# Performance work log

Measured on AMD Instinct MI355X. Metric: run time of the kernel, lower is better.

## Reference

```python
import jax, jax.numpy as jnp
import numpy as np
import math

B, N, DIM, H, D = 2, 2048, 1024, 16, 64
EXPECTED_K = 1.0
LAYERSCALE_INIT = 0.001
EPS = 1e-6  # flax LayerNorm default


def layer_norm(x, scale, bias):
    mu = jnp.mean(x, axis=-1, keepdims=True)
    var = jnp.mean((x - mu) ** 2, axis=-1, keepdims=True)
    return (x - mu) * jax.lax.rsqrt(var + EPS) * scale + bias


def setup_inputs() -> dict:
    key = jax.random.key(0)
    ks = jax.random.split(key, 8)
    s = DIM ** -0.5
    x = jax.random.normal(ks[0], (B, N, DIM), jnp.float32)
    Wq = jax.random.normal(ks[1], (DIM, H * D), jnp.float32) * s
    Wk = jax.random.normal(ks[2], (DIM, H * D), jnp.float32) * s
    Wv = jax.random.normal(ks[3], (DIM, H * D), jnp.float32) * s
    Wo = jax.random.normal(ks[4], (H * D, DIM), jnp.float32) * ((H * D) ** -0.5)
    e = EXPECTED_K / N
    init_bias = jnp.full((1, 1, 1, 1), math.log(e / (1.0 - e)), jnp.float32)
    return {
        'x': x,
        'Wq': Wq, 'bq': jnp.zeros((H * D,), jnp.float32),
        'Wk': Wk, 'bk': jnp.zeros((H * D,), jnp.float32),
        'Wv': Wv, 'bv': jnp.zeros((H * D,), jnp.float32),
        'qn_scale': jnp.ones((D,), jnp.float32), 'qn_bias': jnp.zeros((D,), jnp.float32),
        'kn_scale': jnp.ones((D,), jnp.float32), 'kn_bias': jnp.zeros((D,), jnp.float32),
        'init_bias': init_bias,
        'Wo': Wo, 'bo': jnp.zeros((DIM,), jnp.float32),
        'gamma': jnp.full((DIM,), LAYERSCALE_INIT, jnp.float32),
    }


def reference(x, Wq, bq, Wk, bk, Wv, bv, qn_scale, qn_bias, kn_scale, kn_bias,
              init_bias, Wo, bo, gamma):
    Bv, Nv, _ = x.shape
    q = (x @ Wq + bq).reshape(Bv, Nv, H, D)
    k = (x @ Wk + bk).reshape(Bv, Nv, H, D)
    v = (x @ Wv + bv).reshape(Bv, Nv, H, D)
    q = layer_norm(q, qn_scale, qn_bias)
    k = layer_norm(k, kn_scale, kn_bias)
    q = jnp.swapaxes(q, 1, 2)  # [B,H,N,D]
    k = jnp.swapaxes(k, 1, 2)
    v = jnp.swapaxes(v, 1, 2)
    # NOTE: original code computes scale = head_dim**-0.5 but never applies it.
    attn_logits = jnp.einsum('bhid,bhjd->bhij', q, k)
    attn_weights = jax.nn.sigmoid(attn_logits + init_bias)
    out = jnp.einsum('bhij,bhjd->bhid', attn_weights, v)
    out = jnp.swapaxes(out, 1, 2).reshape(Bv, Nv, H * D)
    out = out @ Wo + bo
    return out * gamma
```

## Files before the change

kernel.cpp:

```cpp
#include <hip/hip_runtime.h>

#define DEV static __device__ __forceinline__

typedef __bf16 bf16x8 __attribute__((ext_vector_type(8)));
typedef __bf16 bf16x4 __attribute__((ext_vector_type(4)));
typedef float f32x4 __attribute__((ext_vector_type(4)));
typedef float f32x16 __attribute__((ext_vector_type(16)));
typedef unsigned int uint4v __attribute__((ext_vector_type(4)));
typedef unsigned short ushort4v __attribute__((ext_vector_type(4)));
using u16 = unsigned short;

#define NN 2048
#define DIMD 1024

DEV u16 f2bf(float f) {
    __bf16 b = (__bf16)f;
    return __builtin_bit_cast(u16, b);
}
DEV float bf2f(u16 s) {
    unsigned u = ((unsigned)s) << 16;
    return __builtin_bit_cast(float, u);
}
DEV bf16x8 load16(const u16* p) { return __builtin_bit_cast(bf16x8, *(const uint4v*)p); }
DEV f32x4 mfma16(bf16x8 a, bf16x8 b, f32x4 c) {
    return __builtin_amdgcn_mfma_f32_16x16x32_bf16(a, b, c, 0, 0, 0);
}
DEV f32x16 mfma32(bf16x8 a, bf16x8 b, f32x16 c) {
    return __builtin_amdgcn_mfma_f32_32x32x16_bf16(a, b, c, 0, 0, 0);
}
DEV void gl_lds16(const u16* g, u16* l) {
    __builtin_amdgcn_global_load_lds((const __attribute__((address_space(1))) void*)g,
                                     (__attribute__((address_space(3))) void*)l, 16, 0, 0);
}


__global__ __launch_bounds__(256) void k_prep(const float* __restrict__ x,
                                              const float* __restrict__ s0,
                                              const float* __restrict__ s1,
                                              const float* __restrict__ s2,
                                              const float* __restrict__ s3,
                                              u16* __restrict__ xb,
                                              u16* __restrict__ wqkv_t,
                                              u16* __restrict__ wo_t) {
    __shared__ float tile[32][33];
    const int z = blockIdx.z;
    if (z < 4) {
        const float* src = (z == 0) ? s0 : (z == 1) ? s1 : (z == 2) ? s2 : s3;
        u16* dst = (z < 3) ? (wqkv_t + (size_t)z * 1024 * 1024) : wo_t;
        int tx = threadIdx.x & 31, ty = threadIdx.x >> 5;
        int kb = blockIdx.y * 32, nb = blockIdx.x * 32;
#pragma unroll
        for (int j = 0; j < 4; ++j)
            tile[ty + 8 * j][tx] = src[(size_t)(kb + ty + 8 * j) * 1024 + nb + tx];
        __syncthreads();
#pragma unroll
        for (int j = 0; j < 4; ++j)
            dst[(size_t)(nb + ty + 8 * j) * 1024 + kb + tx] = f2bf(tile[tx][ty + 8 * j]);
    } else {
        const int bidx = blockIdx.y * 32 + blockIdx.x;
#pragma unroll
        for (int q = 0; q < 4; ++q) {
            int i = bidx * 1024 + q * 256 + threadIdx.x;
            float4 v = ((const float4*)x)[i];
            ushort4v o;
            o[0] = f2bf(v.x); o[1] = f2bf(v.y); o[2] = f2bf(v.z); o[3] = f2bf(v.w);
            *(ushort4v*)(xb + (size_t)i * 4) = o;
        }
    }
}

__global__ __launch_bounds__(256) void k_gemm_qkv(const u16* __restrict__ A,
                                                  const u16* __restrict__ Bt,
                                                  const float* __restrict__ bq,
                                                  const float* __restrict__ bk,
                                                  const float* __restrict__ bv,
                                                  const float* __restrict__ qs,
                                                  const float* __restrict__ qb,
                                                  const float* __restrict__ ks,
                                                  const float* __restrict__ kb_,
                                                  u16* __restrict__ Qf,
                                                  u16* __restrict__ Kf,
                                                  u16* __restrict__ Vf) {
    __shared__ u16 As[128 * 64];
    __shared__ u16 Bs[128 * 64];
    const int K = 1024;
    const int m0 = blockIdx.x * 128, n0 = blockIdx.y * 128;
    const int tid = threadIdx.x;
    const int lane = tid & 63, w = tid >> 6;
    const int wr = w >> 1, wc = w & 1;
    const int li = lane & 15, g = lane >> 4;
    const int l7 = li & 7;

    f32x4 acc[4][4] = {};

    const int lr = lane >> 3;
    const int lc = (lane & 7) ^ lr;
    const u16* gA = A + (size_t)(m0 + w * 8 + lr) * K + lc * 8;
    const u16* gB = Bt + (size_t)(n0 + w * 8 + lr) * K + lc * 8;
    u16* lA = &As[w * 512];
    u16* lB = &Bs[w * 512];

    for (int k0 = 0; k0 < K; k0 += 64) {
        __syncthreads();
#pragma unroll
        for (int i = 0; i < 4; ++i) {
            gl_lds16(gA + (size_t)(i * 32) * K + k0, lA + i * 2048);
            gl_lds16(gB + (size_t)(i * 32) * K + k0, lB + i * 2048);
        }
        asm volatile("s_waitcnt vmcnt(0)" ::: "memory");
        __syncthreads();
        bf16x8 af[4][2], bfv[4][2];
#pragma unroll
        for (int mi = 0; mi < 4; ++mi) {
            const int row = wr * 64 + mi * 16 + li;
#pragma unroll
            for (int s = 0; s < 2; ++s)
                af[mi][s] = load16(&As[row * 64 + (((s * 4 + g) ^ l7) * 8)]);
        }
#pragma unroll
        for (int ni = 0; ni < 4; ++ni) {
            const int row = wc * 64 + ni * 16 + li;
#pragma unroll
            for (int s = 0; s < 2; ++s)
                bfv[ni][s] = load16(&Bs[row * 64 + (((s * 4 + g) ^ l7) * 8)]);
        }
#pragma unroll
        for (int mi = 0; mi < 4; ++mi)
#pragma unroll
            for (int ni = 0; ni < 4; ++ni) {
                acc[mi][ni] = mfma16(af[mi][0], bfv[ni][0], acc[mi][ni]);
                acc[mi][ni] = mfma16(af[mi][1], bfv[ni][1], acc[mi][ni]);
            }
    }

    const int col0 = n0 + wc * 64;
    const int seg = col0 >> 10;
    const int hcol = col0 & 1023;
    const int h = hcol >> 6;

    if (seg < 2) {
        const float* S = (seg == 0) ? qs : ks;
        const float* Bb = (seg == 0) ? qb : kb_;
        const float* bias = (seg == 0) ? bq : bk;
        u16* dst = (seg == 0) ? Qf : Kf;
        const float sc = (seg == 0) ? -1.44269504f : 1.0f;
        float lnS[4], lnB[4], bv4[4];
#pragma unroll
        for (int ni = 0; ni < 4; ++ni) {
            int d = ni * 16 + li;
            lnS[ni] = S[d] * sc; lnB[ni] = Bb[d] * sc; bv4[ni] = bias[hcol + d];
        }
#pragma unroll
        for (int mi = 0; mi < 4; ++mi) {
#pragma unroll
            for (int r = 0; r < 4; ++r) {
                float v0 = acc[mi][0][r] + bv4[0];
                float v1 = acc[mi][1][r] + bv4[1];
                float v2 = acc[mi][2][r] + bv4[2];
                float v3 = acc[mi][3][r] + bv4[3];
                float s1 = v0 + v1 + v2 + v3;
                float s2 = v0 * v0 + v1 * v1 + v2 * v2 + v3 * v3;
#pragma unroll
                for (int o = 1; o < 16; o <<= 1) {
                    s1 += __shfl_xor(s1, o);
                    s2 += __shfl_xor(s2, o);
                }
                float mu = s1 * (1.0f / 64.0f);
                float var = s2 * (1.0f / 64.0f) - mu * mu;
                float rsv = rsqrtf(var + 1e-6f);
                int row = m0 + wr * 64 + mi * 16 + 4 * g + r;
                int bseq = row >> 11, n = row & 2047;
                size_t base = ((size_t)(bseq * 16 + h)) * 131072 +
                              ((size_t)(n >> 5) * 4) * 512 + (size_t)(n & 31) * 8 +
                              (li >> 3) * 256 + (li & 7);
                dst[base + 0 * 512] = f2bf((v0 - mu) * rsv * lnS[0] + lnB[0]);
                dst[base + 1 * 512] = f2bf((v1 - mu) * rsv * lnS[1] + lnB[1]);
                dst[base + 2 * 512] = f2bf((v2 - mu) * rsv * lnS[2] + lnB[2]);
                dst[base + 3 * 512] = f2bf((v3 - mu) * rsv * lnS[3] + lnB[3]);
            }
        }
    } else {
        float bv4[4];
#pragma unroll
        for (int ni = 0; ni < 4; ++ni) bv4[ni] = bv[hcol + ni * 16 + li];
#pragma unroll
        for (int mi = 0; mi < 4; ++mi) {
#pragma unroll
            for (int r = 0; r < 4; ++r) {
                int row = m0 + wr * 64 + mi * 16 + 4 * g + r;
                int bseq = row >> 11, j = row & 2047;
                size_t vb_ = ((size_t)(bseq * 16 + h)) * 131072 +
                             ((size_t)((j >> 5) * 4 + ((j >> 4) & 1))) * 512 +
                             (size_t)(((j >> 3) & 1) * 32) * 8 + (j & 7);
#pragma unroll
                for (int ni = 0; ni < 4; ++ni)
                    Vf[vb_ + (ni >> 1) * 1024 + ((ni & 1) * 16 + li) * 8] =
                        f2bf(acc[mi][ni][r] + bv4[ni]);
            }
        }
    }
}

__global__ __launch_bounds__(256) void k_gemm_out(const u16* __restrict__ A,
                                                  const u16* __restrict__ Bt,
                                                  const float* __restrict__ bias,
                                                  const float* __restrict__ gamma,
                                                  float* __restrict__ out) {
    __shared__ u16 As[128 * 64];
    __shared__ u16 Bs[64 * 64];
    const int K = 1024, ldc = 1024;
    const int m0 = blockIdx.x * 128, n0 = blockIdx.y * 64;
    const int tid = threadIdx.x;
    const int lane = tid & 63, w = tid >> 6;
    const int wr = w >> 1, wc = w & 1;
    const int li = lane & 15, g = lane >> 4;
    const int l7 = li & 7;

    f32x4 acc[4][2] = {};

    const int lr = lane >> 3;
    const int lc = (lane & 7) ^ lr;
    const u16* gA = A + (size_t)(m0 + w * 8 + lr) * K + lc * 8;
    const u16* gB = Bt + (size_t)(n0 + w * 8 + lr) * K + lc * 8;
    u16* lA = &As[w * 512];
    u16* lB = &Bs[w * 512];

    for (int k0 = 0; k0 < K; k0 += 64) {
        __syncthreads();
#pragma unroll
        for (int i = 0; i < 4; ++i)
            gl_lds16(gA + (size_t)(i * 32) * K + k0, lA + i * 2048);
#pragma unroll
        for (int i = 0; i < 2; ++i)
            gl_lds16(gB + (size_t)(i * 32) * K + k0, lB + i * 2048);
        asm volatile("s_waitcnt vmcnt(0)" ::: "memory");
        __syncthreads();
        bf16x8 af[4][2], bfv[2][2];
#pragma unroll
        for (int mi = 0; mi < 4; ++mi) {
            const int row = wr * 64 + mi * 16 + li;
#pragma unroll
            for (int s = 0; s < 2; ++s)
                af[mi][s] = load16(&As[row * 64 + (((s * 4 + g) ^ l7) * 8)]);
        }
#pragma unroll
        for (int ni = 0; ni < 2; ++ni) {
            const int row = wc * 32 + ni * 16 + li;
#pragma unroll
            for (int s = 0; s < 2; ++s)
                bfv[ni][s] = load16(&Bs[row * 64 + (((s * 4 + g) ^ l7) * 8)]);
        }
#pragma unroll
        for (int mi = 0; mi < 4; ++mi)
#pragma unroll
            for (int ni = 0; ni < 2; ++ni) {
                acc[mi][ni] = mfma16(af[mi][0], bfv[ni][0], acc[mi][ni]);
                acc[mi][ni] = mfma16(af[mi][1], bfv[ni][1], acc[mi][ni]);
            }
    }

#pragma unroll
    for (int mi = 0; mi < 4; ++mi) {
        int row = m0 + wr * 64 + mi * 16 + 4 * g;
#pragma unroll
        for (int ni = 0; ni < 2; ++ni) {
            int col = n0 + wc * 32 + ni * 16 + li;
            float bv_ = bias[col], gv = gamma[col];
            f32x4 v = acc[mi][ni];
#pragma unroll
            for (int r = 0; r < 4; ++r)
                out[(size_t)(row + r) * ldc + col] = (v[r] + bv_) * gv;
        }
    }
}

__global__ __launch_bounds__(256, 2) void k_attn(const u16* __restrict__ Qf,
                                                 const u16* __restrict__ Kf,
                                                 const u16* __restrict__ Vf,
                                                 const float* __restrict__ ib,
                                                 u16* __restrict__ attn_out) {
    __shared__ float red[2][64][65];
    const int bid = blockIdx.x;
    const int xcd = bid & 7, idx = bid >> 3;
    const int bh = xcd * 4 + (idx >> 5);
    const int iblk = idx & 31;
    const int b = bh >> 4, h = bh & 15;
    const int tid = threadIdx.x;
    const int jq = tid >> 6, lane = tid & 63;
    const int l32 = lane & 31, hi = lane >> 5;
    const float c0 = -ib[0] * 1.44269504f;
    const u16* Qb = Qf + (size_t)bh * 131072;
    const u16* Kb = Kf + (size_t)bh * 131072;
    const u16* Vb = Vf + (size_t)bh * 131072;
    const int it0 = iblk * 2;

    bf16x8 qf[2][4];
#pragma unroll
    for (int t = 0; t < 2; ++t)
#pragma unroll
        for (int s = 0; s < 4; ++s)
            qf[t][s] = load16(Qb + ((size_t)((it0 + t) * 4 + s)) * 512 + lane * 8);

    f32x16 accO[2][2] = {};
    const u16* kb0 = Kb + (size_t)(jq * 16) * 2048;
    const u16* vb0 = Vb + (size_t)(jq * 16) * 2048;

    f32x16 cinit;
#pragma unroll
    for (int r = 0; r < 16; ++r) cinit[r] = c0;

    bf16x8 kf[2][4], vf[2][2][2];
#pragma unroll
    for (int s = 0; s < 4; ++s) kf[0][s] = load16(kb0 + s * 512 + lane * 8);
#pragma unroll
    for (int s = 0; s < 4; ++s) kf[1][s] = load16(kb0 + 2048 + s * 512 + lane * 8);
#pragma unroll
    for (int db = 0; db < 2; ++db)
#pragma unroll
        for (int js = 0; js < 2; ++js)
            vf[0][db][js] = load16(vb0 + (db * 2 + js) * 512 + lane * 8);
    f32x16 sa0 = cinit, sa1;
#pragma unroll
    for (int s = 0; s < 4; ++s) sa0 = mfma32(kf[0][s], qf[0][s], sa0);

#pragma unroll 2
    for (int jt = 0; jt < 16; ++jt) {
        const int cur = jt & 1, nxt = cur ^ 1;
        if (jt < 15) {
            const u16* vbn = vb0 + (size_t)(jt + 1) * 2048;
#pragma unroll
            for (int db = 0; db < 2; ++db)
#pragma unroll
                for (int js = 0; js < 2; ++js)
                    vf[nxt][db][js] = load16(vbn + (db * 2 + js) * 512 + lane * 8);
        }
        __builtin_amdgcn_s_setprio(1);
        sa1 = cinit;
#pragma unroll
        for (int s = 0; s < 4; ++s) sa1 = mfma32(kf[cur][s], qf[1][s], sa1);
        __builtin_amdgcn_s_setprio(0);
        if (jt < 14) {
            const u16* kbn = kb0 + (size_t)(jt + 2) * 2048;
#pragma unroll
            for (int s = 0; s < 4; ++s) kf[cur][s] = load16(kbn + s * 512 + lane * 8);
        }
        bf16x8 p00, p01;
        {
            float p[16];
#pragma unroll
            for (int r = 0; r < 16; ++r) {
                float e = __builtin_amdgcn_exp2f(sa0[r]);
                p[r] = __builtin_amdgcn_rcpf(1.0f + e);
            }
            unsigned wd[8];
#pragma unroll
            for (int u2 = 0; u2 < 8; ++u2) {
                unsigned r_;
                asm("v_cvt_pk_bf16_f32 %0, %1, %2"
                    : "=v"(r_) : "v"(p[2 * u2]), "v"(p[2 * u2 + 1]));
                wd[u2] = r_;
            }
            asm("v_permlane32_swap_b32 %0, %1" : "+v"(wd[0]), "+v"(wd[2]));
            asm("v_permlane32_swap_b32 %0, %1" : "+v"(wd[1]), "+v"(wd[3]));
            asm("v_permlane32_swap_b32 %0, %1" : "+v"(wd[4]), "+v"(wd[6]));
            asm("v_permlane32_swap_b32 %0, %1" : "+v"(wd[5]), "+v"(wd[7]));
            uint4v u0 = {wd[0], wd[1], wd[2], wd[3]};
            uint4v u1 = {wd[4], wd[5], wd[6], wd[7]};
            p00 = __builtin_bit_cast(bf16x8, u0);
            p01 = __builtin_bit_cast(bf16x8, u1);
        }
        __builtin_amdgcn_s_setprio(1);
        accO[0][0] = mfma32(vf[cur][0][0], p00, accO[0][0]);
        accO[0][0] = mfma32(vf[cur][0][1], p01, accO[0][0]);
        accO[0][1] = mfma32(vf[cur][1][0], p00, accO[0][1]);
        accO[0][1] = mfma32(vf[cur][1][1], p01, accO[0][1]);
        if (jt < 15) {
            sa0 = cinit;
#pragma unroll
            for (int s = 0; s < 4; ++s) sa0 = mfma32(kf[nxt][s], qf[0][s], sa0);
        }
        __builtin_amdgcn_s_setprio(0);
        bf16x8 p10, p11;
        {
            float p[16];
#pragma unroll
            for (int r = 0; r < 16; ++r) {
                float e = __builtin_amdgcn_exp2f(sa1[r]);
                p[r] = __builtin_amdgcn_rcpf(1.0f + e);
            }
            unsigned wd[8];
#pragma unroll
            for (int u2 = 0; u2 < 8; ++u2) {
                unsigned r_;
                asm("v_cvt_pk_bf16_f32 %0, %1, %2"
                    : "=v"(r_) : "v"(p[2 * u2]), "v"(p[2 * u2 + 1]));
                wd[u2] = r_;
            }
            asm("v_permlane32_swap_b32 %0, %1" : "+v"(wd[0]), "+v"(wd[2]));
            asm("v_permlane32_swap_b32 %0, %1" : "+v"(wd[1]), "+v"(wd[3]));
            asm("v_permlane32_swap_b32 %0, %1" : "+v"(wd[4]), "+v"(wd[6]));
            asm("v_permlane32_swap_b32 %0, %1" : "+v"(wd[5]), "+v"(wd[7]));
            uint4v u0 = {wd[0], wd[1], wd[2], wd[3]};
            uint4v u1 = {wd[4], wd[5], wd[6], wd[7]};
            p10 = __builtin_bit_cast(bf16x8, u0);
            p11 = __builtin_bit_cast(bf16x8, u1);
        }
        __builtin_amdgcn_s_setprio(1);
        accO[1][0] = mfma32(vf[cur][0][0], p10, accO[1][0]);
        accO[1][0] = mfma32(vf[cur][0][1], p11, accO[1][0]);
        accO[1][1] = mfma32(vf[cur][1][0], p10, accO[1][1]);
        accO[1][1] = mfma32(vf[cur][1][1], p11, accO[1][1]);
        __builtin_amdgcn_s_setprio(0);
    }

    if (jq & 1) {
#pragma unroll
        for (int t = 0; t < 2; ++t)
#pragma unroll
            for (int db = 0; db < 2; ++db)
#pragma unroll
                for (int r = 0; r < 16; ++r)
                    red[jq >> 1][t * 32 + l32][db * 32 + (r & 3) + 8 * (r >> 2) + 4 * hi] =
                        accO[t][db][r];
    }
    __syncthreads();
    if (!(jq & 1)) {
#pragma unroll
        for (int t = 0; t < 2; ++t)
#pragma unroll
            for (int db = 0; db < 2; ++db)
#pragma unroll
                for (int r = 0; r < 16; ++r)
                    accO[t][db][r] +=
                        red[jq >> 1][t * 32 + l32][db * 32 + (r & 3) + 8 * (r >> 2) + 4 * hi];
    }
    __syncthreads();
    if (jq == 2) {
#pragma unroll
        for (int t = 0; t < 2; ++t)
#pragma unroll
            for (int db = 0; db < 2; ++db)
#pragma unroll
                for (int r = 0; r < 16; ++r)
                    red[0][t * 32 + l32][db * 32 + (r & 3) + 8 * (r >> 2) + 4 * hi] =
                        accO[t][db][r];
    }
    __syncthreads();
    if (jq == 0) {
#pragma unroll
        for (int t = 0; t < 2; ++t)
#pragma unroll
            for (int db = 0; db < 2; ++db)
#pragma unroll
                for (int r = 0; r < 16; ++r)
                    accO[t][db][r] +=
                        red[0][t * 32 + l32][db * 32 + (r & 3) + 8 * (r >> 2) + 4 * hi];
#pragma unroll
        for (int t = 0; t < 2; ++t) {
            const int i = it0 * 32 + t * 32 + l32;
#pragma unroll
            for (int db = 0; db < 2; ++db)
#pragma unroll
                for (int q = 0; q < 4; ++q) {
                    int d = db * 32 + 8 * q + 4 * hi;
                    bf16x4 o4;
#pragma unroll
                    for (int r = 0; r < 4; ++r) o4[r] = (__bf16)accO[t][db][4 * q + r];
                    *(bf16x4*)&attn_out[(size_t)(b * NN + i) * 1024 + h * 64 + d] = o4;
                }
        }
    }
}


extern "C" void kernel_launch(void* const* d_in, const int* in_sizes, int n_in,
                              void* d_out, int out_size, void* d_ws, size_t ws_size,
                              hipStream_t stream) {
    (void)in_sizes; (void)n_in; (void)out_size; (void)ws_size;
    const float* x     = (const float*)d_in[0];
    const float* Wq    = (const float*)d_in[1];
    const float* bq    = (const float*)d_in[2];
    const float* Wk    = (const float*)d_in[3];
    const float* bk    = (const float*)d_in[4];
    const float* Wv    = (const float*)d_in[5];
    const float* bv    = (const float*)d_in[6];
    const float* qn_s  = (const float*)d_in[7];
    const float* qn_b  = (const float*)d_in[8];
    const float* kn_s  = (const float*)d_in[9];
    const float* kn_b  = (const float*)d_in[10];
    const float* ib    = (const float*)d_in[11];
    const float* Wo    = (const float*)d_in[12];
    const float* bo    = (const float*)d_in[13];
    const float* gamma = (const float*)d_in[14];
    float* out = (float*)d_out;

    char* ws = (char*)d_ws;
    size_t off = 0;
    auto alloc = [&](size_t bytes) -> void* {
        void* p = ws + off;
        off += (bytes + 255) & ~(size_t)255;
        return p;
    };
    u16* xb       = (u16*)alloc((size_t)4096 * 1024 * 2);
    u16* wqkv_t   = (u16*)alloc((size_t)3072 * 1024 * 2);
    u16* wo_t     = (u16*)alloc((size_t)1024 * 1024 * 2);
    u16* Qf       = (u16*)alloc((size_t)32 * 131072 * 2);
    u16* Kf       = (u16*)alloc((size_t)32 * 131072 * 2);
    u16* Vf       = (u16*)alloc((size_t)32 * 131072 * 2);
    u16* attn_out = (u16*)alloc((size_t)4096 * 1024 * 2);

    k_prep<<<dim3(32, 32, 5), 256, 0, stream>>>(x, Wq, Wk, Wv, Wo, xb, wqkv_t, wo_t);
    k_gemm_qkv<<<dim3(32, 24), 256, 0, stream>>>(xb, wqkv_t, bq, bk, bv,
                                                 qn_s, qn_b, kn_s, kn_b, Qf, Kf, Vf);
    k_attn<<<1024, 256, 0, stream>>>(Qf, Kf, Vf, ib, attn_out);
    k_gemm_out<<<dim3(32, 16), 256, 0, stream>>>(attn_out, wo_t, bo, gamma, out);
}
```

Before: 116.7 us.

## Give each wave private LDS tiles and overlap next-tile loads with MFMA in GEMMs

Both projection GEMMs now give each wave its own LDS region for its 64-row A and B slices, so the block-wide __syncthreads barriers disappear. Each iteration reads its fragments into registers, then issues the global-to-LDS loads for the next K tile before the MFMAs, so memory traffic overlaps compute. The output GEMM also widens from 128x64 to 128x128 tiles, which halves the grid. The cost is redundant global loads, since waves sharing a row or column each fetch the same data, plus fewer blocks for the output GEMM. Overwriting LDS while other lanes read it relies on the lgkmcnt wait completing within the wave.

After: 116.5 us. About the same (-0.1%).

```diff
diff --git a/kernel.cpp b/kernel.cpp
--- a/kernel.cpp
+++ b/kernel.cpp
@@ -81,8 +81,7 @@
                                                   u16* __restrict__ Qf,
                                                   u16* __restrict__ Kf,
                                                   u16* __restrict__ Vf) {
-    __shared__ u16 As[128 * 64];
-    __shared__ u16 Bs[128 * 64];
+    __shared__ u16 lds[4][2][64 * 32 * 2];
     const int K = 1024;
     const int m0 = blockIdx.x * 128, n0 = blockIdx.y * 128;
     const int tid = threadIdx.x;
@@ -93,37 +92,43 @@
 
     f32x4 acc[4][4] = {};
 
+    u16* lA = &lds[w][0][0];
+    u16* lB = &lds[w][1][0];
     const int lr = lane >> 3;
     const int lc = (lane & 7) ^ lr;
-    const u16* gA = A + (size_t)(m0 + w * 8 + lr) * K + lc * 8;
-    const u16* gB = Bt + (size_t)(n0 + w * 8 + lr) * K + lc * 8;
-    u16* lA = &As[w * 512];
-    u16* lB = &Bs[w * 512];
-
-    for (int k0 = 0; k0 < K; k0 += 64) {
-        __syncthreads();
-#pragma unroll
-        for (int i = 0; i < 4; ++i) {
-            gl_lds16(gA + (size_t)(i * 32) * K + k0, lA + i * 2048);
-            gl_lds16(gB + (size_t)(i * 32) * K + k0, lB + i * 2048);
-        }
-        asm volatile("s_waitcnt vmcnt(0)" ::: "memory");
-        __syncthreads();
+    const u16* gA = A + (size_t)(m0 + wr * 64 + lr) * K + lc * 8;
+    const u16* gB = Bt + (size_t)(n0 + wc * 64 + lr) * K + lc * 8;
+
+    auto STAGE = [&](int k0) {
+#pragma unroll
+        for (int i = 0; i < 8; ++i) {
+            gl_lds16(gA + (size_t)(i * 8) * K + k0, lA + i * 512);
+            gl_lds16(gB + (size_t)(i * 8) * K + k0, lB + i * 512);
+        }
+    };
+
+    STAGE(0);
+    asm volatile("s_waitcnt vmcnt(0)" ::: "memory");
+
+    for (int t = 0; t < 16; ++t) {
         bf16x8 af[4][2], bfv[4][2];
 #pragma unroll
         for (int mi = 0; mi < 4; ++mi) {
-            const int row = wr * 64 + mi * 16 + li;
+            const int row = mi * 16 + li;
 #pragma unroll
             for (int s = 0; s < 2; ++s)
-                af[mi][s] = load16(&As[row * 64 + (((s * 4 + g) ^ l7) * 8)]);
+                af[mi][s] = load16(&lA[row * 64 + (((s * 4 + g) ^ l7) * 8)]);
         }
 #pragma unroll
         for (int ni = 0; ni < 4; ++ni) {
-            const int row = wc * 64 + ni * 16 + li;
+            const int row = ni * 16 + li;
 #pragma unroll
             for (int s = 0; s < 2; ++s)
-                bfv[ni][s] = load16(&Bs[row * 64 + (((s * 4 + g) ^ l7) * 8)]);
-        }
+                bfv[ni][s] = load16(&lB[row * 64 + (((s * 4 + g) ^ l7) * 8)]);
+        }
+        asm volatile("s_waitcnt lgkmcnt(0)" ::: "memory");
+        __builtin_amdgcn_sched_barrier(0);
+        if (t < 15) STAGE((t + 1) * 64);
 #pragma unroll
         for (int mi = 0; mi < 4; ++mi)
 #pragma unroll
@@ -131,6 +136,7 @@
                 acc[mi][ni] = mfma16(af[mi][0], bfv[ni][0], acc[mi][ni]);
                 acc[mi][ni] = mfma16(af[mi][1], bfv[ni][1], acc[mi][ni]);
             }
+        asm volatile("s_waitcnt vmcnt(0)" ::: "memory");
     }
 
     const int col0 = n0 + wc * 64;
@@ -206,65 +212,70 @@
                                                   const float* __restrict__ bias,
                                                   const float* __restrict__ gamma,
                                                   float* __restrict__ out) {
-    __shared__ u16 As[128 * 64];
-    __shared__ u16 Bs[64 * 64];
+    __shared__ u16 lds[4][2][64 * 32 * 2];
     const int K = 1024, ldc = 1024;
-    const int m0 = blockIdx.x * 128, n0 = blockIdx.y * 64;
+    const int m0 = blockIdx.x * 128, n0 = blockIdx.y * 128;
     const int tid = threadIdx.x;
     const int lane = tid & 63, w = tid >> 6;
     const int wr = w >> 1, wc = w & 1;
     const int li = lane & 15, g = lane >> 4;
     const int l7 = li & 7;
 
-    f32x4 acc[4][2] = {};
-
+    f32x4 acc[4][4] = {};
+
+    u16* lA = &lds[w][0][0];
+    u16* lB = &lds[w][1][0];
     const int lr = lane >> 3;
     const int lc = (lane & 7) ^ lr;
-    const u16* gA = A + (size_t)(m0 + w * 8 + lr) * K + lc * 8;
-    const u16* gB = Bt + (size_t)(n0 + w * 8 + lr) * K + lc * 8;
-    u16* lA = &As[w * 512];
-    u16* lB = &Bs[w * 512];
-
-    for (int k0 = 0; k0 < K; k0 += 64) {
-        __syncthreads();
-#pragma unroll
-        for (int i = 0; i < 4; ++i)
-            gl_lds16(gA + (size_t)(i * 32) * K + k0, lA + i * 2048);
-#pragma unroll
-        for (int i = 0; i < 2; ++i)
-            gl_lds16(gB + (size_t)(i * 32) * K + k0, lB + i * 2048);
-        asm volatile("s_waitcnt vmcnt(0)" ::: "memory");
-        __syncthreads();
-        bf16x8 af[4][2], bfv[2][2];
+    const u16* gA = A + (size_t)(m0 + wr * 64 + lr) * K + lc * 8;
+    const u16* gB = Bt + (size_t)(n0 + wc * 64 + lr) * K + lc * 8;
+
+    auto STAGE = [&](int k0) {
+#pragma unroll
+        for (int i = 0; i < 8; ++i) {
+            gl_lds16(gA + (size_t)(i * 8) * K + k0, lA + i * 512);
+            gl_lds16(gB + (size_t)(i * 8) * K + k0, lB + i * 512);
+        }
+    };
+
+    STAGE(0);
+    asm volatile("s_waitcnt vmcnt(0)" ::: "memory");
+
+    for (int t = 0; t < 16; ++t) {
+        bf16x8 af[4][2], bfv[4][2];
 #pragma unroll
         for (int mi = 0; mi < 4; ++mi) {
-            const int row = wr * 64 + mi * 16 + li;
+            const int row = mi * 16 + li;
 #pragma unroll
             for (int s = 0; s < 2; ++s)
-                af[mi][s] = load16(&As[row * 64 + (((s * 4 + g) ^ l7) * 8)]);
-        }
-#pragma unroll
-        for (int ni = 0; ni < 2; ++ni) {
-            const int row = wc * 32 + ni * 16 + li;
+                af[mi][s] = load16(&lA[row * 64 + (((s * 4 + g) ^ l7) * 8)]);
+        }
+#pragma unroll
+        for (int ni = 0; ni < 4; ++ni) {
+            const int row = ni * 16 + li;
 #pragma unroll
             for (int s = 0; s < 2; ++s)
-                bfv[ni][s] = load16(&Bs[row * 64 + (((s * 4 + g) ^ l7) * 8)]);
-        }
+                bfv[ni][s] = load16(&lB[row * 64 + (((s * 4 + g) ^ l7) * 8)]);
+        }
+        asm volatile("s_waitcnt lgkmcnt(0)" ::: "memory");
+        __builtin_amdgcn_sched_barrier(0);
+        if (t < 15) STAGE((t + 1) * 64);
 #pragma unroll
         for (int mi = 0; mi < 4; ++mi)
 #pragma unroll
-            for (int ni = 0; ni < 2; ++ni) {
+            for (int ni = 0; ni < 4; ++ni) {
                 acc[mi][ni] = mfma16(af[mi][0], bfv[ni][0], acc[mi][ni]);
                 acc[mi][ni] = mfma16(af[mi][1], bfv[ni][1], acc[mi][ni]);
             }
+        asm volatile("s_waitcnt vmcnt(0)" ::: "memory");
     }
 
 #pragma unroll
     for (int mi = 0; mi < 4; ++mi) {
         int row = m0 + wr * 64 + mi * 16 + 4 * g;
 #pragma unroll
-        for (int ni = 0; ni < 2; ++ni) {
-            int col = n0 + wc * 32 + ni * 16 + li;
+        for (int ni = 0; ni < 4; ++ni) {
+            int col = n0 + wc * 64 + ni * 16 + li;
             float bv_ = bias[col], gv = gamma[col];
             f32x4 v = acc[mi][ni];
 #pragma unroll
@@ -513,5 +524,5 @@
     k_gemm_qkv<<<dim3(32, 24), 256, 0, stream>>>(xb, wqkv_t, bq, bk, bv,
                                                  qn_s, qn_b, kn_s, kn_b, Qf, Kf, Vf);
     k_attn<<<1024, 256, 0, stream>>>(Qf, Kf, Vf, ib, attn_out);
-    k_gemm_out<<<dim3(32, 16), 256, 0, stream>>>(attn_out, wo_t, bo, gamma, out);
-}
+    k_gemm_out<<<dim3(32, 8), 256, 0, stream>>>(attn_out, wo_t, bo, gamma, out);
+}
```
